# Optimization experiments

Measured on AMD Instinct MI355X. Metric: run time of the kernel, lower is better.

## Reference

```python
import jax, jax.numpy as jnp
import numpy as np

NUM_GRAPHS = 1000


def gcn_conv(x, src, dst, n_nodes, W, b):
    """PyG GCNConv: symmetric normalization with self-loops, then scatter-add."""
    # self-loops already appended to src/dst by caller
    deg = jax.ops.segment_sum(jnp.ones_like(dst, dtype=x.dtype), dst, num_segments=n_nodes)
    dinv = jnp.where(deg > 0, jax.lax.rsqrt(deg), 0.0)
    norm = dinv[src] * dinv[dst]                      # [E+N]
    h = x @ W.T                                       # [N, out]
    msg = h[src] * norm[:, None]                      # gather + scale
    out = jax.ops.segment_sum(msg, dst, num_segments=n_nodes)
    return out + b


def setup_inputs() -> dict:
    key = jax.random.key(0)
    ks = jax.random.split(key, 9)
    N, E = 100000, 1600000
    x = jax.random.normal(ks[0], (N, 32), dtype=jnp.float32)
    edge_index = jax.random.randint(ks[1], (2, E), 0, N, dtype=jnp.int64)
    batch = jnp.sort(jax.random.randint(ks[2], (N,), 0, NUM_GRAPHS, dtype=jnp.int64))
    # parameters (Glorot-ish scale)
    W1 = jax.random.normal(ks[3], (16, 32), dtype=jnp.float32) * (1.0 / np.sqrt(32))
    b1 = jnp.zeros((16,), dtype=jnp.float32)
    W2 = jax.random.normal(ks[4], (16, 16), dtype=jnp.float32) * (1.0 / np.sqrt(16))
    b2 = jnp.zeros((16,), dtype=jnp.float32)
    Wl = jax.random.normal(ks[5], (5, 16), dtype=jnp.float32) * (1.0 / np.sqrt(16))
    bl = jnp.zeros((5,), dtype=jnp.float32)
    return {"x": x, "edge_index": edge_index, "batch": batch,
            "W1": W1, "b1": b1, "W2": W2, "b2": b2, "Wl": Wl, "bl": bl}


def reference(x, edge_index, batch, W1, b1, W2, b2, Wl, bl):
    n_nodes = x.shape[0]
    loops = jnp.arange(n_nodes, dtype=edge_index.dtype)
    src = jnp.concatenate([edge_index[0], loops])
    dst = jnp.concatenate([edge_index[1], loops])

    h = gcn_conv(x, src, dst, n_nodes, W1, b1)
    h = jax.nn.relu(h)
    h = gcn_conv(h, src, dst, n_nodes, W2, b2)

    # global mean pool over graphs
    sums = jax.ops.segment_sum(h, batch, num_segments=NUM_GRAPHS)
    cnts = jax.ops.segment_sum(jnp.ones((n_nodes,), dtype=h.dtype), batch, num_segments=NUM_GRAPHS)
    pooled = sums / jnp.maximum(cnts, 1.0)[:, None]   # [G, 16]

    logits = pooled @ Wl.T + bl                       # [G, 5]
    return jax.nn.softmax(logits, axis=-1)
```

## Files before the change

### kernel.cpp

```cpp
#include <hip/hip_runtime.h>
#include <hip/hip_fp16.h>
#include <math.h>

#define NG 1000
#define NPN 512
#define PSH 9
#define MAXPART 256
#define K1BLK 256

__global__ void __launch_bounds__(256) hist_kernel(const int* __restrict__ dst,
                                                   int* __restrict__ bhist,
                                                   int4* __restrict__ zero4, int z4,
                                                   int E, int CH) {
    __shared__ int h[MAXPART];
    int b = blockIdx.x, t = threadIdx.x;
    h[t] = 0;
    int gid = b * 256 + t;
    if (gid < z4) zero4[gid] = make_int4(0, 0, 0, 0);
    __syncthreads();
    int beg = b * CH, end = min(E, beg + CH);
    for (int e = beg + t; e < end; e += 256) atomicAdd(&h[dst[e] >> PSH], 1);
    __syncthreads();
    bhist[t * K1BLK + b] = h[t];
}

__global__ void __launch_bounds__(256) scanA_kernel(const int* __restrict__ bhist,
                                                    int* __restrict__ gbase,
                                                    int* __restrict__ pcnt, int NPART) {
    int wid = blockIdx.x * 4 + (threadIdx.x >> 6);
    int lane = threadIdx.x & 63;
    if (wid >= NPART) return;
    int base = wid * K1BLK + lane * 4;
    int v0 = bhist[base + 0], v1 = bhist[base + 1];
    int v2 = bhist[base + 2], v3 = bhist[base + 3];
    int s = v0 + v1 + v2 + v3;
    int incl = s;
    for (int off = 1; off < 64; off <<= 1) {
        int u = __shfl_up(incl, off);
        if (lane >= off) incl += u;
    }
    int run = incl - s;
    gbase[base + 0] = run;            run += v0;
    gbase[base + 1] = run;            run += v1;
    gbase[base + 2] = run;            run += v2;
    gbase[base + 3] = run;
    if (lane == 63) pcnt[wid] = incl;
}

__global__ void __launch_bounds__(64) scanB_kernel(const int* __restrict__ pcnt,
                                                   int* __restrict__ poff,
                                                   int* __restrict__ rowptr,
                                                   int NPART, int N, int E) {
    int lane = threadIdx.x;
    int v[4];
    int s = 0;
#pragma unroll
    for (int k = 0; k < 4; k++) {
        int idx = lane * 4 + k;
        v[k] = (idx < NPART) ? pcnt[idx] : 0;
        s += v[k];
    }
    int incl = s;
    for (int off = 1; off < 64; off <<= 1) {
        int u = __shfl_up(incl, off);
        if (lane >= off) incl += u;
    }
    int run = incl - s;
#pragma unroll
    for (int k = 0; k < 4; k++) {
        int idx = lane * 4 + k;
        if (idx < NPART) poff[idx] = run;
        run += v[k];
    }
    int grand = __shfl(incl, 63);
    if (lane == 0) { poff[NPART] = grand; rowptr[N] = E; }
}

__global__ void __launch_bounds__(256) scatter_kernel(const int* __restrict__ src,
                                                      const int* __restrict__ dst,
                                                      const int* __restrict__ poff,
                                                      const int* __restrict__ gbase,
                                                      int* __restrict__ ibuf,
                                                      int E, int CH, int NPART) {
    __shared__ int cur[MAXPART];
    int b = blockIdx.x, t = threadIdx.x;
    if (t < NPART) cur[t] = poff[t] + gbase[t * K1BLK + b];
    __syncthreads();
    int beg = b * CH, end = min(E, beg + CH);
    for (int e = beg + t; e < end; e += 256) {
        int s = src[e], d = dst[e];
        int p = d >> PSH;
        int pos = atomicAdd(&cur[p], 1);
        ibuf[pos] = ((d & (NPN - 1)) << 17) | s;
    }
}

__global__ void __launch_bounds__(256) part_kernel(const int* __restrict__ poff,
                                                   const int* __restrict__ ibuf,
                                                   int* __restrict__ csr,
                                                   int* __restrict__ rowptr,
                                                   float* __restrict__ dinv,
                                                   const float* __restrict__ X,
                                                   const float* __restrict__ W1,
                                                   __half* __restrict__ A1h, int N) {
    __shared__ int h[NPN];
    __shared__ int ex[NPN];
    __shared__ int cur[NPN];
    __shared__ int sm[256];
    __shared__ float sW1[512];
    int p = blockIdx.x, t = threadIdx.x;
    int base = p * NPN;
    for (int k = t; k < NPN; k += 256) h[k] = 0;
    sW1[t] = W1[t];
    sW1[t + 256] = W1[t + 256];
    __syncthreads();
    int ebeg = poff[p], eend = poff[p + 1];
    for (int e = ebeg + t; e < eend; e += 256) atomicAdd(&h[ibuf[e] >> 17], 1);
    __syncthreads();
    int a0 = h[2 * t], a1 = h[2 * t + 1];
    int s = a0 + a1;
    sm[t] = s;
    __syncthreads();
    for (int o = 1; o < 256; o <<= 1) {
        int u = (t >= o) ? sm[t - o] : 0;
        __syncthreads();
        sm[t] += u;
        __syncthreads();
    }
    int exc = sm[t] - s;
    ex[2 * t] = exc;          cur[2 * t] = exc;
    ex[2 * t + 1] = exc + a0; cur[2 * t + 1] = exc + a0;
    __syncthreads();
    for (int k = t; k < NPN; k += 256) {
        int n = base + k;
        if (n < N) {
            rowptr[n] = ebeg + ex[k];
            dinv[n] = rsqrtf((float)h[k] + 1.0f);
        }
    }
    for (int e = ebeg + t; e < eend; e += 256) {
        int w = ibuf[e];
        int ln = w >> 17;
        int pos = ebeg + atomicAdd(&cur[ln], 1);
        csr[pos] = w & 0x1FFFF;
    }
    for (int k = t; k < NPN; k += 256) {
        int n = base + k;
        if (n >= N) continue;
        float dd = rsqrtf((float)h[k] + 1.0f);
        float xv[32];
        const float4* xp = (const float4*)(X + (size_t)n * 32);
#pragma unroll
        for (int qq = 0; qq < 8; qq++) {
            float4 v = xp[qq];
            xv[4*qq+0] = v.x; xv[4*qq+1] = v.y; xv[4*qq+2] = v.z; xv[4*qq+3] = v.w;
        }
        union { __half2 h2[8]; uint4 u4[2]; } pk;
#pragma unroll
        for (int j2 = 0; j2 < 8; j2++) {
            float o[2];
#pragma unroll
            for (int jj = 0; jj < 2; jj++) {
                int j = j2 * 2 + jj;
                float a = 0.f;
#pragma unroll
                for (int kk = 0; kk < 32; kk++) a += xv[kk] * sW1[j * 32 + kk];
                o[jj] = a * dd;
            }
            pk.h2[j2] = __floats2half2_rn(o[0], o[1]);
        }
        uint4* yp = (uint4*)(A1h + (size_t)n * 16);
        yp[0] = pk.u4[0];
        yp[1] = pk.u4[1];
    }
}

__device__ __forceinline__ void add8(float* a, uint4 v) {
    float2 f;
    f = __half22float2(*(const __half2*)&v.x); a[0] += f.x; a[1] += f.y;
    f = __half22float2(*(const __half2*)&v.y); a[2] += f.x; a[3] += f.y;
    f = __half22float2(*(const __half2*)&v.z); a[4] += f.x; a[5] += f.y;
    f = __half22float2(*(const __half2*)&v.w); a[6] += f.x; a[7] += f.y;
}

__global__ void __launch_bounds__(256) agg1_kernel(
    const int* __restrict__ rowptr, const int* __restrict__ csr,
    const float* __restrict__ dinv, const __half* __restrict__ A1h,
    const float* __restrict__ b1, const float* __restrict__ W2,
    __half* __restrict__ A2h, int N) {
    __shared__ float sW2[256];
    __shared__ float sb1[16];
    __shared__ float tile[128][17];
    int t = threadIdx.x;
    int team = t >> 1, q = t & 1;
    int node = blockIdx.x * 128 + team;
    sW2[t] = W2[t];
    if (t < 16) sb1[t] = b1[t];
    __syncthreads();
    const uint4* H4 = (const uint4*)A1h;
    float dd = 0.f;
    if (node < N) {
        dd = dinv[node];
        float acc[8] = {0.f,0.f,0.f,0.f,0.f,0.f,0.f,0.f};
        add8(acc, H4[(size_t)node * 2 + q]);
        int e = rowptr[node], end = rowptr[node + 1];
        for (; e + 3 < end; e += 4) {
            int s0 = csr[e], s1 = csr[e+1], s2 = csr[e+2], s3 = csr[e+3];
            uint4 g0 = H4[(size_t)s0 * 2 + q];
            uint4 g1 = H4[(size_t)s1 * 2 + q];
            uint4 g2 = H4[(size_t)s2 * 2 + q];
            uint4 g3 = H4[(size_t)s3 * 2 + q];
            add8(acc, g0); add8(acc, g1); add8(acc, g2); add8(acc, g3);
        }
        for (; e < end; e++) add8(acc, H4[(size_t)csr[e] * 2 + q]);
#pragma unroll
        for (int j = 0; j < 8; j++)
            tile[team][q * 8 + j] = fmaxf(acc[j] * dd + sb1[q * 8 + j], 0.f);
    }
    __syncthreads();
    if (node < N) {
        float o[8];
#pragma unroll
        for (int jj = 0; jj < 8; jj++) {
            int j = q * 8 + jj;
            float a = 0.f;
#pragma unroll
            for (int k = 0; k < 16; k++) a += tile[team][k] * sW2[j * 16 + k];
            o[jj] = a * dd;
        }
        uint4 ov;
        ((__half2*)&ov)[0] = __floats2half2_rn(o[0], o[1]);
        ((__half2*)&ov)[1] = __floats2half2_rn(o[2], o[3]);
        ((__half2*)&ov)[2] = __floats2half2_rn(o[4], o[5]);
        ((__half2*)&ov)[3] = __floats2half2_rn(o[6], o[7]);
        ((uint4*)A2h)[(size_t)node * 2 + q] = ov;
    }
}

__global__ void __launch_bounds__(256) agg2_kernel(
    const int* __restrict__ rowptr, const int* __restrict__ csr,
    const float* __restrict__ dinv, const __half* __restrict__ A2h,
    const int* __restrict__ batch, float* __restrict__ pooled,
    float* __restrict__ cnt, int N) {
    __shared__ float tile[128][17];
    __shared__ int gb[128];
    int t = threadIdx.x;
    int team = t >> 1, q = t & 1;
    int base = blockIdx.x * 128;
    int node = base + team;
    if (t < 128) {
        int n = base + t;
        gb[t] = (n < N) ? batch[n] : -1;
    }
    const uint4* H4 = (const uint4*)A2h;
    if (node < N) {
        float dd = dinv[node];
        float acc[8] = {0.f,0.f,0.f,0.f,0.f,0.f,0.f,0.f};
        add8(acc, H4[(size_t)node * 2 + q]);
        int e = rowptr[node], end = rowptr[node + 1];
        for (; e + 3 < end; e += 4) {
            int s0 = csr[e], s1 = csr[e+1], s2 = csr[e+2], s3 = csr[e+3];
            uint4 g0 = H4[(size_t)s0 * 2 + q];
            uint4 g1 = H4[(size_t)s1 * 2 + q];
            uint4 g2 = H4[(size_t)s2 * 2 + q];
            uint4 g3 = H4[(size_t)s3 * 2 + q];
            add8(acc, g0); add8(acc, g1); add8(acc, g2); add8(acc, g3);
        }
        for (; e < end; e++) add8(acc, H4[(size_t)csr[e] * 2 + q]);
#pragma unroll
        for (int j = 0; j < 8; j++) tile[team][q * 8 + j] = acc[j] * dd;
    }
    __syncthreads();
    int nmax = N - base; if (nmax > 128) nmax = 128;
    if (t < 16 && nmax > 0) {
        int c = t;
        int g = gb[0];
        float a = 0.f, k = 0.f;
        for (int n = 0; n < nmax; n++) {
            int gi = gb[n];
            if (gi != g) {
                atomicAdd(&pooled[(size_t)g * 16 + c], a);
                if (c == 0) atomicAdd(&cnt[g], k);
                a = 0.f; k = 0.f; g = gi;
            }
            a += tile[n][c];
            k += 1.f;
        }
        atomicAdd(&pooled[(size_t)g * 16 + c], a);
        if (c == 0) atomicAdd(&cnt[g], k);
    }
}

__global__ void head_kernel(const float* __restrict__ pooled, const float* __restrict__ cnt,
                            const float* __restrict__ b2, const float* __restrict__ Wl,
                            const float* __restrict__ bl, float* __restrict__ out) {
    int g = blockIdx.x * blockDim.x + threadIdx.x;
    if (g >= NG) return;
    float c = cnt[g];
    c = c > 1.0f ? c : 1.0f;
    float inv = 1.0f / c;
    float p[16];
#pragma unroll
    for (int j = 0; j < 16; j++) p[j] = pooled[(size_t)g * 16 + j] * inv + b2[j];
    float logits[5], m = -INFINITY;
#pragma unroll
    for (int r = 0; r < 5; r++) {
        float a = bl[r];
#pragma unroll
        for (int j = 0; j < 16; j++) a += p[j] * Wl[r * 16 + j];
        logits[r] = a;
        m = fmaxf(m, a);
    }
    float s = 0.f;
#pragma unroll
    for (int r = 0; r < 5; r++) { logits[r] = expf(logits[r] - m); s += logits[r]; }
    float is = 1.0f / s;
#pragma unroll
    for (int r = 0; r < 5; r++) out[(size_t)g * 5 + r] = logits[r] * is;
}

static inline size_t rnd16b(size_t bytes) { return (bytes + 15) & ~(size_t)15; }

extern "C" void kernel_launch(void* const* d_in, const int* in_sizes, int n_in,
                              void* d_out, int out_size, void* d_ws, size_t ws_size,
                              hipStream_t stream) {
    const float* x     = (const float*)d_in[0];
    const int*   edge  = (const int*)d_in[1];
    const int*   batch = (const int*)d_in[2];
    const float* W1    = (const float*)d_in[3];
    const float* b1    = (const float*)d_in[4];
    const float* W2    = (const float*)d_in[5];
    const float* b2    = (const float*)d_in[6];
    const float* Wl    = (const float*)d_in[7];
    const float* bl    = (const float*)d_in[8];

    const int N = in_sizes[0] / 32;
    const int E = in_sizes[1] / 2;
    const int* src = edge;
    const int* dst = edge + E;

    const int NPART = (N + NPN - 1) / NPN;
    const int CH = (E + K1BLK - 1) / K1BLK;

    char* ws = (char*)d_ws;
    size_t off = 0;
    float*    pooled = (float*)(ws + off);    off += rnd16b((size_t)NG * 16 * 4);
    float*    cnt    = (float*)(ws + off);    off += rnd16b((size_t)NG * 4);
    size_t zbytes = off;
    int*      poff   = (int*)(ws + off);      off += rnd16b((size_t)(MAXPART + 1) * 4);
    int*      pcnt   = (int*)(ws + off);      off += rnd16b((size_t)MAXPART * 4);
    int*      rowptr = (int*)(ws + off);      off += rnd16b((size_t)(N + 1) * 4);
    float*    dinv   = (float*)(ws + off);    off += rnd16b((size_t)N * 4);
    int*      bhist  = (int*)(ws + off);      off += rnd16b((size_t)K1BLK * MAXPART * 4);
    int*      gbase  = (int*)(ws + off);      off += rnd16b((size_t)K1BLK * MAXPART * 4);
    int*      ibuf   = (int*)(ws + off);      off += rnd16b((size_t)E * 4);
    int*      csr    = (int*)(ws + off);      off += rnd16b((size_t)E * 4);
    __half*   A1h    = (__half*)(ws + off);   off += rnd16b((size_t)N * 16 * 2);
    __half*   A2h    = (__half*)(ws + off);   off += rnd16b((size_t)N * 16 * 2);

    int z4 = (int)(zbytes / 16);

    hist_kernel<<<K1BLK, 256, 0, stream>>>(dst, bhist, (int4*)d_ws, z4, E, CH);
    scanA_kernel<<<(NPART + 3) / 4, 256, 0, stream>>>(bhist, gbase, pcnt, NPART);
    scanB_kernel<<<1, 64, 0, stream>>>(pcnt, poff, rowptr, NPART, N, E);
    scatter_kernel<<<K1BLK, 256, 0, stream>>>(src, dst, poff, gbase, ibuf, E, CH, NPART);
    part_kernel<<<NPART, 256, 0, stream>>>(poff, ibuf, csr, rowptr, dinv, x, W1, A1h, N);

    int gAgg = (N + 127) / 128;
    agg1_kernel<<<gAgg, 256, 0, stream>>>(rowptr, csr, dinv, A1h, b1, W2, A2h, N);
    agg2_kernel<<<gAgg, 256, 0, stream>>>(rowptr, csr, dinv, A2h, batch, pooled, cnt, N);
    head_kernel<<<(NG + 255) / 256, 256, 0, stream>>>(pooled, cnt, b2, Wl, bl, (float*)d_out);
}
```

Baseline: 103.1 us.

## Fuse all GCN stages into one cooperative persistent kernel with grid syncs

Replaces the eight separate kernel launches with a single cooperative kernel of 256 blocks that runs histogram, scans, scatter, CSR build, both aggregations, pooling and the head, separated by grid-wide syncs. Degree normalization is recomputed from rowptr inline instead of reading a dinv array. The aim is to remove launch gaps and inter-kernel drain. The trade-off is that the aggregation phases now use only 256 persistent blocks looping over strips, which may lower latency hiding for the gather-heavy phases, and grid.sync adds its own cost. Falls back to the old multi-kernel path if cooperative launch is unavailable.

```diff
diff --git a/kernel.cpp b/kernel.cpp
--- a/kernel.cpp
+++ b/kernel.cpp
@@ -1,12 +1,312 @@
 #include <hip/hip_runtime.h>
+#include <hip/hip_cooperative_groups.h>
 #include <hip/hip_fp16.h>
 #include <math.h>
+
+namespace cg = cooperative_groups;
 
 #define NG 1000
 #define NPN 512
 #define PSH 9
 #define MAXPART 256
 #define K1BLK 256
+#define NBLK 256
+#define NTHR 256
+
+__device__ __forceinline__ void add8(float* a, uint4 v) {
+    float2 f;
+    f = __half22float2(*(const __half2*)&v.x); a[0] += f.x; a[1] += f.y;
+    f = __half22float2(*(const __half2*)&v.y); a[2] += f.x; a[3] += f.y;
+    f = __half22float2(*(const __half2*)&v.z); a[4] += f.x; a[5] += f.y;
+    f = __half22float2(*(const __half2*)&v.w); a[6] += f.x; a[7] += f.y;
+}
+
+struct GParams {
+    const float* x; const int* src; const int* dst; const int* batch;
+    const float* W1; const float* b1; const float* W2; const float* b2;
+    const float* Wl; const float* bl; float* out;
+    float* pooled; float* cnt; int* poff; int* rowptr; int* pcnt;
+    int* bhist; int* gbase; int* ibuf; int* csr;
+    __half* A1h; __half* A2h;
+    int N, E, NPART, CH, z4;
+};
+
+__global__ void __launch_bounds__(NTHR) mega_kernel(GParams P) {
+    cg::grid_group grid = cg::this_grid();
+    __shared__ __align__(16) char smem[10368];
+    int b = blockIdx.x, t = threadIdx.x;
+
+    {
+        int4* z = (int4*)P.pooled;
+        for (int i = b * NTHR + t; i < P.z4; i += NBLK * NTHR) z[i] = make_int4(0,0,0,0);
+        int* h = (int*)smem;
+        h[t] = 0;
+        __syncthreads();
+        int beg = b * P.CH, end = min(P.E, beg + P.CH);
+        for (int e = beg + t; e < end; e += NTHR) atomicAdd(&h[P.dst[e] >> PSH], 1);
+        __syncthreads();
+        if (t < P.NPART) P.bhist[t * NBLK + b] = h[t];
+    }
+    grid.sync();
+    {
+        int wid = b * (NTHR / 64) + (t >> 6);
+        int lane = t & 63;
+        if (wid < P.NPART) {
+            int base = wid * NBLK + lane * 4;
+            int v0 = P.bhist[base + 0], v1 = P.bhist[base + 1];
+            int v2 = P.bhist[base + 2], v3 = P.bhist[base + 3];
+            int s = v0 + v1 + v2 + v3;
+            int incl = s;
+            for (int off = 1; off < 64; off <<= 1) {
+                int u = __shfl_up(incl, off);
+                if (lane >= off) incl += u;
+            }
+            int run = incl - s;
+            P.gbase[base + 0] = run;  run += v0;
+            P.gbase[base + 1] = run;  run += v1;
+            P.gbase[base + 2] = run;  run += v2;
+            P.gbase[base + 3] = run;
+            if (lane == 63) P.pcnt[wid] = incl;
+        }
+    }
+    grid.sync();
+    if (b == 0 && t < 64) {
+        int lane = t;
+        int v[4];
+        int s = 0;
+#pragma unroll
+        for (int k = 0; k < 4; k++) {
+            int idx = lane * 4 + k;
+            v[k] = (idx < P.NPART) ? P.pcnt[idx] : 0;
+            s += v[k];
+        }
+        int incl = s;
+        for (int off = 1; off < 64; off <<= 1) {
+            int u = __shfl_up(incl, off);
+            if (lane >= off) incl += u;
+        }
+        int run = incl - s;
+#pragma unroll
+        for (int k = 0; k < 4; k++) {
+            int idx = lane * 4 + k;
+            if (idx < P.NPART) P.poff[idx] = run;
+            run += v[k];
+        }
+        int grand = __shfl(incl, 63);
+        if (lane == 0) { P.poff[P.NPART] = grand; P.rowptr[P.N] = P.E; }
+    }
+    grid.sync();
+    {
+        int* cur = (int*)smem;
+        if (t < P.NPART) cur[t] = P.poff[t] + P.gbase[t * NBLK + b];
+        __syncthreads();
+        int beg = b * P.CH, end = min(P.E, beg + P.CH);
+        for (int e = beg + t; e < end; e += NTHR) {
+            int s = P.src[e], d = P.dst[e];
+            int p = d >> PSH;
+            int pos = atomicAdd(&cur[p], 1);
+            P.ibuf[pos] = ((d & (NPN - 1)) << 17) | s;
+        }
+        __syncthreads();
+    }
+    grid.sync();
+    if (b < P.NPART) {
+        int p = b;
+        int* h    = (int*)smem;
+        int* ex   = h + NPN;
+        int* cur2 = ex + NPN;
+        int* sm   = cur2 + NPN;
+        float* sW1 = (float*)(sm + 256);
+        int base = p * NPN;
+        for (int k = t; k < NPN; k += NTHR) h[k] = 0;
+        sW1[t] = P.W1[t];
+        sW1[t + 256] = P.W1[t + 256];
+        __syncthreads();
+        int ebeg = P.poff[p], eend = P.poff[p + 1];
+        for (int e = ebeg + t; e < eend; e += NTHR) atomicAdd(&h[P.ibuf[e] >> 17], 1);
+        __syncthreads();
+        int a0 = h[2 * t], a1 = h[2 * t + 1];
+        int s = a0 + a1;
+        sm[t] = s;
+        __syncthreads();
+        for (int o = 1; o < 256; o <<= 1) {
+            int u = (t >= o) ? sm[t - o] : 0;
+            __syncthreads();
+            sm[t] += u;
+            __syncthreads();
+        }
+        int exc = sm[t] - s;
+        ex[2 * t] = exc;           cur2[2 * t] = exc;
+        ex[2 * t + 1] = exc + a0;  cur2[2 * t + 1] = exc + a0;
+        __syncthreads();
+        for (int k = t; k < NPN; k += NTHR) {
+            int n = base + k;
+            if (n < P.N) P.rowptr[n] = ebeg + ex[k];
+        }
+        for (int e = ebeg + t; e < eend; e += NTHR) {
+            int w = P.ibuf[e];
+            int ln = w >> 17;
+            int pos = ebeg + atomicAdd(&cur2[ln], 1);
+            P.csr[pos] = w & 0x1FFFF;
+        }
+        for (int k = t; k < NPN; k += NTHR) {
+            int n = base + k;
+            if (n >= P.N) continue;
+            float dd = rsqrtf((float)h[k] + 1.0f);
+            float xv[32];
+            const float4* xp = (const float4*)(P.x + (size_t)n * 32);
+#pragma unroll
+            for (int qq = 0; qq < 8; qq++) {
+                float4 v = xp[qq];
+                xv[4*qq+0] = v.x; xv[4*qq+1] = v.y; xv[4*qq+2] = v.z; xv[4*qq+3] = v.w;
+            }
+            union { __half2 h2[8]; uint4 u4[2]; } pk;
+#pragma unroll
+            for (int j2 = 0; j2 < 8; j2++) {
+                float o[2];
+#pragma unroll
+                for (int jj = 0; jj < 2; jj++) {
+                    int j = j2 * 2 + jj;
+                    float a = 0.f;
+#pragma unroll
+                    for (int kk = 0; kk < 32; kk++) a += xv[kk] * sW1[j * 32 + kk];
+                    o[jj] = a * dd;
+                }
+                pk.h2[j2] = __floats2half2_rn(o[0], o[1]);
+            }
+            uint4* yp = (uint4*)(P.A1h + (size_t)n * 16);
+            yp[0] = pk.u4[0];
+            yp[1] = pk.u4[1];
+        }
+    }
+    grid.sync();
+    {
+        float* sW2 = (float*)smem;
+        float* sb1 = sW2 + 256;
+        float (*tile)[17] = (float (*)[17])(sb1 + 16);
+        sW2[t] = P.W2[t];
+        if (t < 16) sb1[t] = P.b1[t];
+        __syncthreads();
+        int strips = (P.N + 127) / 128;
+        const uint4* H4 = (const uint4*)P.A1h;
+        int team = t >> 1, q = t & 1;
+        for (int sblk = b; sblk < strips; sblk += NBLK) {
+            int node = sblk * 128 + team;
+            float dd = 0.f;
+            if (node < P.N) {
+                int e = P.rowptr[node], end = P.rowptr[node + 1];
+                dd = rsqrtf((float)(end - e) + 1.0f);
+                float acc[8] = {0.f,0.f,0.f,0.f,0.f,0.f,0.f,0.f};
+                add8(acc, H4[(size_t)node * 2 + q]);
+                for (; e + 3 < end; e += 4) {
+                    int s0 = P.csr[e], s1 = P.csr[e+1], s2 = P.csr[e+2], s3 = P.csr[e+3];
+                    uint4 g0 = H4[(size_t)s0 * 2 + q];
+                    uint4 g1 = H4[(size_t)s1 * 2 + q];
+                    uint4 g2 = H4[(size_t)s2 * 2 + q];
+                    uint4 g3 = H4[(size_t)s3 * 2 + q];
+                    add8(acc, g0); add8(acc, g1); add8(acc, g2); add8(acc, g3);
+                }
+                for (; e < end; e++) add8(acc, H4[(size_t)P.csr[e] * 2 + q]);
+#pragma unroll
+                for (int j = 0; j < 8; j++)
+                    tile[team][q * 8 + j] = fmaxf(acc[j] * dd + sb1[q * 8 + j], 0.f);
+            }
+            __syncthreads();
+            if (node < P.N) {
+                float o[8];
+#pragma unroll
+                for (int jj = 0; jj < 8; jj++) {
+                    int j = q * 8 + jj;
+                    float a = 0.f;
+#pragma unroll
+                    for (int k = 0; k < 16; k++) a += tile[team][k] * sW2[j * 16 + k];
+                    o[jj] = a * dd;
+                }
+                uint4 ov;
+                ((__half2*)&ov)[0] = __floats2half2_rn(o[0], o[1]);
+                ((__half2*)&ov)[1] = __floats2half2_rn(o[2], o[3]);
+                ((__half2*)&ov)[2] = __floats2half2_rn(o[4], o[5]);
+                ((__half2*)&ov)[3] = __floats2half2_rn(o[6], o[7]);
+                ((uint4*)P.A2h)[(size_t)node * 2 + q] = ov;
+            }
+            __syncthreads();
+        }
+    }
+    grid.sync();
+    {
+        float (*tile)[17] = (float (*)[17])smem;
+        int* gb = (int*)(smem + 128 * 17 * 4);
+        int strips = (P.N + 127) / 128;
+        const uint4* H4 = (const uint4*)P.A2h;
+        int team = t >> 1, q = t & 1;
+        for (int sblk = b; sblk < strips; sblk += NBLK) {
+            int base2 = sblk * 128;
+            int node = base2 + team;
+            if (t < 128) gb[t] = (base2 + t < P.N) ? P.batch[base2 + t] : -1;
+            if (node < P.N) {
+                int e = P.rowptr[node], end = P.rowptr[node + 1];
+                float dd = rsqrtf((float)(end - e) + 1.0f);
+                float acc[8] = {0.f,0.f,0.f,0.f,0.f,0.f,0.f,0.f};
+                add8(acc, H4[(size_t)node * 2 + q]);
+                for (; e + 3 < end; e += 4) {
+                    int s0 = P.csr[e], s1 = P.csr[e+1], s2 = P.csr[e+2], s3 = P.csr[e+3];
+                    uint4 g0 = H4[(size_t)s0 * 2 + q];
+                    uint4 g1 = H4[(size_t)s1 * 2 + q];
+                    uint4 g2 = H4[(size_t)s2 * 2 + q];
+                    uint4 g3 = H4[(size_t)s3 * 2 + q];
+                    add8(acc, g0); add8(acc, g1); add8(acc, g2); add8(acc, g3);
+                }
+                for (; e < end; e++) add8(acc, H4[(size_t)P.csr[e] * 2 + q]);
+#pragma unroll
+                for (int j = 0; j < 8; j++) tile[team][q * 8 + j] = acc[j] * dd;
+            }
+            __syncthreads();
+            int nmax = P.N - base2; if (nmax > 128) nmax = 128;
+            if (t < 16 && nmax > 0) {
+                int c = t;
+                int g = gb[0];
+                float a = 0.f, k = 0.f;
+                for (int n = 0; n < nmax; n++) {
+                    int gi = gb[n];
+                    if (gi != g) {
+                        atomicAdd(&P.pooled[(size_t)g * 16 + c], a);
+                        if (c == 0) atomicAdd(&P.cnt[g], k);
+                        a = 0.f; k = 0.f; g = gi;
+                    }
+                    a += tile[n][c];
+                    k += 1.f;
+                }
+                atomicAdd(&P.pooled[(size_t)g * 16 + c], a);
+                if (c == 0) atomicAdd(&P.cnt[g], k);
+            }
+            __syncthreads();
+        }
+    }
+    grid.sync();
+    for (int g = b * NTHR + t; g < NG; g += NBLK * NTHR) {
+        float c = P.cnt[g];
+        c = c > 1.0f ? c : 1.0f;
+        float inv = 1.0f / c;
+        float pv[16];
+#pragma unroll
+        for (int j = 0; j < 16; j++) pv[j] = P.pooled[(size_t)g * 16 + j] * inv + P.b2[j];
+        float logits[5], m = -INFINITY;
+#pragma unroll
+        for (int r = 0; r < 5; r++) {
+            float a = P.bl[r];
+#pragma unroll
+            for (int j = 0; j < 16; j++) a += pv[j] * P.Wl[r * 16 + j];
+            logits[r] = a;
+            m = fmaxf(m, a);
+        }
+        float s = 0.f;
+#pragma unroll
+        for (int r = 0; r < 5; r++) { logits[r] = expf(logits[r] - m); s += logits[r]; }
+        float is = 1.0f / s;
+#pragma unroll
+        for (int r = 0; r < 5; r++) P.out[(size_t)g * 5 + r] = logits[r] * is;
+    }
+}
 
 __global__ void __launch_bounds__(256) hist_kernel(const int* __restrict__ dst,
                                                    int* __restrict__ bhist,
@@ -175,14 +475,6 @@
     }
 }
 
-__device__ __forceinline__ void add8(float* a, uint4 v) {
-    float2 f;
-    f = __half22float2(*(const __half2*)&v.x); a[0] += f.x; a[1] += f.y;
-    f = __half22float2(*(const __half2*)&v.y); a[2] += f.x; a[3] += f.y;
-    f = __half22float2(*(const __half2*)&v.z); a[4] += f.x; a[5] += f.y;
-    f = __half22float2(*(const __half2*)&v.w); a[6] += f.x; a[7] += f.y;
-}
-
 __global__ void __launch_bounds__(256) agg1_kernel(
     const int* __restrict__ rowptr, const int* __restrict__ csr,
     const float* __restrict__ dinv, const __half* __restrict__ A1h,
@@ -340,7 +632,6 @@
     const int* dst = edge + E;
 
     const int NPART = (N + NPN - 1) / NPN;
-    const int CH = (E + K1BLK - 1) / K1BLK;
 
     char* ws = (char*)d_ws;
     size_t off = 0;
@@ -360,12 +651,36 @@
 
     int z4 = (int)(zbytes / 16);
 
+    int dev = 0, coop = 0, nCU = 0, maxB = 0;
+    hipGetDevice(&dev);
+    hipDeviceGetAttribute(&coop, hipDeviceAttributeCooperativeLaunch, dev);
+    hipDeviceGetAttribute(&nCU, hipDeviceAttributeMultiprocessorCount, dev);
+    hipError_t occ = hipOccupancyMaxActiveBlocksPerMultiprocessor(&maxB, (const void*)mega_kernel, NTHR, 0);
+    bool canCoop = (coop == 1) && (occ == hipSuccess) && ((long)maxB * nCU >= NBLK);
+    if (canCoop) {
+        GParams P;
+        P.x = x; P.src = src; P.dst = dst; P.batch = batch;
+        P.W1 = W1; P.b1 = b1; P.W2 = W2; P.b2 = b2; P.Wl = Wl; P.bl = bl;
+        P.out = (float*)d_out;
+        P.pooled = pooled; P.cnt = cnt; P.poff = poff; P.rowptr = rowptr; P.pcnt = pcnt;
+        P.bhist = bhist; P.gbase = gbase; P.ibuf = ibuf; P.csr = csr;
+        P.A1h = A1h; P.A2h = A2h;
+        P.N = N; P.E = E; P.NPART = NPART;
+        P.CH = (E + NBLK - 1) / NBLK;
+        P.z4 = z4;
+        void* kargs[] = { (void*)&P };
+        hipError_t err = hipLaunchCooperativeKernel((const void*)mega_kernel,
+                                                    dim3(NBLK), dim3(NTHR), kargs, 0, stream);
+        if (err == hipSuccess) return;
+        (void)hipGetLastError();
+    }
+
+    const int CH = (E + K1BLK - 1) / K1BLK;
     hist_kernel<<<K1BLK, 256, 0, stream>>>(dst, bhist, (int4*)d_ws, z4, E, CH);
     scanA_kernel<<<(NPART + 3) / 4, 256, 0, stream>>>(bhist, gbase, pcnt, NPART);
     scanB_kernel<<<1, 64, 0, stream>>>(pcnt, poff, rowptr, NPART, N, E);
     scatter_kernel<<<K1BLK, 256, 0, stream>>>(src, dst, poff, gbase, ibuf, E, CH, NPART);
     part_kernel<<<NPART, 256, 0, stream>>>(poff, ibuf, csr, rowptr, dinv, x, W1, A1h, N);
-
     int gAgg = (N + 127) / 128;
     agg1_kernel<<<gAgg, 256, 0, stream>>>(rowptr, csr, dinv, A1h, b1, W2, A2h, N);
     agg2_kernel<<<gAgg, 256, 0, stream>>>(rowptr, csr, dinv, A2h, batch, pooled, cnt, N);
```

New measurement: 103.9 us. About the same (+0.7%).

## Fold partition scan into consumers, derive dinv from rowptr, fuse head via last-block ticket

Applied to the files above, without the earlier changes.

Removes the single-block scanB kernel by having every scatter and part block recompute the partition-offset scan from pcnt redundantly. Drops the dinv array and instead recomputes the inverse square-root degree from rowptr differences in both aggregation kernels. Fuses the pooling head and softmax into agg2 using an atomic done-counter so the last block finishes the work. This removes two kernel launches and some global traffic, at the cost of redundant scan work per block and a serialized tail in one block.

```diff
diff --git a/kernel.cpp b/kernel.cpp
--- a/kernel.cpp
+++ b/kernel.cpp
@@ -47,44 +47,37 @@
     if (lane == 63) pcnt[wid] = incl;
 }
 
-__global__ void __launch_bounds__(64) scanB_kernel(const int* __restrict__ pcnt,
-                                                   int* __restrict__ poff,
-                                                   int* __restrict__ rowptr,
-                                                   int NPART, int N, int E) {
-    int lane = threadIdx.x;
-    int v[4];
-    int s = 0;
-#pragma unroll
-    for (int k = 0; k < 4; k++) {
-        int idx = lane * 4 + k;
-        v[k] = (idx < NPART) ? pcnt[idx] : 0;
-        s += v[k];
-    }
-    int incl = s;
-    for (int off = 1; off < 64; off <<= 1) {
-        int u = __shfl_up(incl, off);
-        if (lane >= off) incl += u;
-    }
-    int run = incl - s;
-#pragma unroll
-    for (int k = 0; k < 4; k++) {
-        int idx = lane * 4 + k;
-        if (idx < NPART) poff[idx] = run;
-        run += v[k];
-    }
-    int grand = __shfl(incl, 63);
-    if (lane == 0) { poff[NPART] = grand; rowptr[N] = E; }
-}
-
 __global__ void __launch_bounds__(256) scatter_kernel(const int* __restrict__ src,
                                                       const int* __restrict__ dst,
-                                                      const int* __restrict__ poff,
+                                                      const int* __restrict__ pcnt,
                                                       const int* __restrict__ gbase,
                                                       int* __restrict__ ibuf,
                                                       int E, int CH, int NPART) {
     __shared__ int cur[MAXPART];
     int b = blockIdx.x, t = threadIdx.x;
-    if (t < NPART) cur[t] = poff[t] + gbase[t * K1BLK + b];
+    if (t < 64) {
+        int lane = t;
+        int v[4];
+        int s = 0;
+#pragma unroll
+        for (int k = 0; k < 4; k++) {
+            int idx = lane * 4 + k;
+            v[k] = (idx < NPART) ? pcnt[idx] : 0;
+            s += v[k];
+        }
+        int incl = s;
+        for (int off = 1; off < 64; off <<= 1) {
+            int u = __shfl_up(incl, off);
+            if (lane >= off) incl += u;
+        }
+        int run = incl - s;
+#pragma unroll
+        for (int k = 0; k < 4; k++) {
+            int idx = lane * 4 + k;
+            if (idx < NPART) cur[idx] = run + gbase[idx * K1BLK + b];
+            run += v[k];
+        }
+    }
     __syncthreads();
     int beg = b * CH, end = min(E, beg + CH);
     for (int e = beg + t; e < end; e += 256) {
@@ -95,26 +88,51 @@
     }
 }
 
-__global__ void __launch_bounds__(256) part_kernel(const int* __restrict__ poff,
+__global__ void __launch_bounds__(256) part_kernel(const int* __restrict__ pcnt,
                                                    const int* __restrict__ ibuf,
                                                    int* __restrict__ csr,
                                                    int* __restrict__ rowptr,
-                                                   float* __restrict__ dinv,
                                                    const float* __restrict__ X,
                                                    const float* __restrict__ W1,
-                                                   __half* __restrict__ A1h, int N) {
+                                                   __half* __restrict__ A1h,
+                                                   int N, int E, int NPART) {
     __shared__ int h[NPN];
     __shared__ int ex[NPN];
     __shared__ int cur[NPN];
     __shared__ int sm[256];
     __shared__ float sW1[512];
+    __shared__ int sEbeg, sEend;
     int p = blockIdx.x, t = threadIdx.x;
     int base = p * NPN;
     for (int k = t; k < NPN; k += 256) h[k] = 0;
     sW1[t] = W1[t];
     sW1[t + 256] = W1[t + 256];
-    __syncthreads();
-    int ebeg = poff[p], eend = poff[p + 1];
+    if (t < 64) {
+        int lane = t;
+        int v[4];
+        int s = 0;
+#pragma unroll
+        for (int k = 0; k < 4; k++) {
+            int idx = lane * 4 + k;
+            v[k] = (idx < NPART) ? pcnt[idx] : 0;
+            s += v[k];
+        }
+        int incl = s;
+        for (int off = 1; off < 64; off <<= 1) {
+            int u = __shfl_up(incl, off);
+            if (lane >= off) incl += u;
+        }
+        int run = incl - s;
+#pragma unroll
+        for (int k = 0; k < 4; k++) {
+            int idx = lane * 4 + k;
+            if (idx == p) { sEbeg = run; sEend = run + v[k]; }
+            run += v[k];
+        }
+    }
+    if (p == 0 && t == 0) rowptr[N] = E;
+    __syncthreads();
+    int ebeg = sEbeg, eend = sEend;
     for (int e = ebeg + t; e < eend; e += 256) atomicAdd(&h[ibuf[e] >> 17], 1);
     __syncthreads();
     int a0 = h[2 * t], a1 = h[2 * t + 1];
@@ -133,10 +151,7 @@
     __syncthreads();
     for (int k = t; k < NPN; k += 256) {
         int n = base + k;
-        if (n < N) {
-            rowptr[n] = ebeg + ex[k];
-            dinv[n] = rsqrtf((float)h[k] + 1.0f);
-        }
+        if (n < N) rowptr[n] = ebeg + ex[k];
     }
     for (int e = ebeg + t; e < eend; e += 256) {
         int w = ibuf[e];
@@ -185,9 +200,8 @@
 
 __global__ void __launch_bounds__(256) agg1_kernel(
     const int* __restrict__ rowptr, const int* __restrict__ csr,
-    const float* __restrict__ dinv, const __half* __restrict__ A1h,
-    const float* __restrict__ b1, const float* __restrict__ W2,
-    __half* __restrict__ A2h, int N) {
+    const __half* __restrict__ A1h, const float* __restrict__ b1,
+    const float* __restrict__ W2, __half* __restrict__ A2h, int N) {
     __shared__ float sW2[256];
     __shared__ float sb1[16];
     __shared__ float tile[128][17];
@@ -200,10 +214,10 @@
     const uint4* H4 = (const uint4*)A1h;
     float dd = 0.f;
     if (node < N) {
-        dd = dinv[node];
+        int e = rowptr[node], end = rowptr[node + 1];
+        dd = rsqrtf((float)(end - e) + 1.0f);
         float acc[8] = {0.f,0.f,0.f,0.f,0.f,0.f,0.f,0.f};
         add8(acc, H4[(size_t)node * 2 + q]);
-        int e = rowptr[node], end = rowptr[node + 1];
         for (; e + 3 < end; e += 4) {
             int s0 = csr[e], s1 = csr[e+1], s2 = csr[e+2], s3 = csr[e+3];
             uint4 g0 = H4[(size_t)s0 * 2 + q];
@@ -239,11 +253,14 @@
 
 __global__ void __launch_bounds__(256) agg2_kernel(
     const int* __restrict__ rowptr, const int* __restrict__ csr,
-    const float* __restrict__ dinv, const __half* __restrict__ A2h,
-    const int* __restrict__ batch, float* __restrict__ pooled,
-    float* __restrict__ cnt, int N) {
+    const __half* __restrict__ A2h, const int* __restrict__ batch,
+    float* __restrict__ pooled, float* __restrict__ cnt,
+    int* __restrict__ done,
+    const float* __restrict__ b2, const float* __restrict__ Wl,
+    const float* __restrict__ bl, float* __restrict__ out, int N) {
     __shared__ float tile[128][17];
     __shared__ int gb[128];
+    __shared__ int sTicket;
     int t = threadIdx.x;
     int team = t >> 1, q = t & 1;
     int base = blockIdx.x * 128;
@@ -254,10 +271,10 @@
     }
     const uint4* H4 = (const uint4*)A2h;
     if (node < N) {
-        float dd = dinv[node];
+        int e = rowptr[node], end = rowptr[node + 1];
+        float dd = rsqrtf((float)(end - e) + 1.0f);
         float acc[8] = {0.f,0.f,0.f,0.f,0.f,0.f,0.f,0.f};
         add8(acc, H4[(size_t)node * 2 + q]);
-        int e = rowptr[node], end = rowptr[node + 1];
         for (; e + 3 < end; e += 4) {
             int s0 = csr[e], s1 = csr[e+1], s2 = csr[e+2], s3 = csr[e+3];
             uint4 g0 = H4[(size_t)s0 * 2 + q];
@@ -289,34 +306,35 @@
         atomicAdd(&pooled[(size_t)g * 16 + c], a);
         if (c == 0) atomicAdd(&cnt[g], k);
     }
-}
-
-__global__ void head_kernel(const float* __restrict__ pooled, const float* __restrict__ cnt,
-                            const float* __restrict__ b2, const float* __restrict__ Wl,
-                            const float* __restrict__ bl, float* __restrict__ out) {
-    int g = blockIdx.x * blockDim.x + threadIdx.x;
-    if (g >= NG) return;
-    float c = cnt[g];
-    c = c > 1.0f ? c : 1.0f;
-    float inv = 1.0f / c;
-    float p[16];
-#pragma unroll
-    for (int j = 0; j < 16; j++) p[j] = pooled[(size_t)g * 16 + j] * inv + b2[j];
-    float logits[5], m = -INFINITY;
-#pragma unroll
-    for (int r = 0; r < 5; r++) {
-        float a = bl[r];
-#pragma unroll
-        for (int j = 0; j < 16; j++) a += p[j] * Wl[r * 16 + j];
-        logits[r] = a;
-        m = fmaxf(m, a);
-    }
-    float s = 0.f;
-#pragma unroll
-    for (int r = 0; r < 5; r++) { logits[r] = expf(logits[r] - m); s += logits[r]; }
-    float is = 1.0f / s;
-#pragma unroll
-    for (int r = 0; r < 5; r++) out[(size_t)g * 5 + r] = logits[r] * is;
+    __threadfence();
+    __syncthreads();
+    if (t == 0) sTicket = atomicAdd(done, 1);
+    __syncthreads();
+    if (sTicket != (int)gridDim.x - 1) return;
+    for (int g = t; g < NG; g += 256) {
+        float c = atomicAdd(&cnt[g], 0.0f);
+        c = c > 1.0f ? c : 1.0f;
+        float inv = 1.0f / c;
+        float pv[16];
+#pragma unroll
+        for (int j = 0; j < 16; j++)
+            pv[j] = atomicAdd(&pooled[(size_t)g * 16 + j], 0.0f) * inv + b2[j];
+        float logits[5], m = -INFINITY;
+#pragma unroll
+        for (int r = 0; r < 5; r++) {
+            float a = bl[r];
+#pragma unroll
+            for (int j = 0; j < 16; j++) a += pv[j] * Wl[r * 16 + j];
+            logits[r] = a;
+            m = fmaxf(m, a);
+        }
+        float s = 0.f;
+#pragma unroll
+        for (int r = 0; r < 5; r++) { logits[r] = expf(logits[r] - m); s += logits[r]; }
+        float is = 1.0f / s;
+#pragma unroll
+        for (int r = 0; r < 5; r++) out[(size_t)g * 5 + r] = logits[r] * is;
+    }
 }
 
 static inline size_t rnd16b(size_t bytes) { return (bytes + 15) & ~(size_t)15; }
@@ -346,11 +364,10 @@
     size_t off = 0;
     float*    pooled = (float*)(ws + off);    off += rnd16b((size_t)NG * 16 * 4);
     float*    cnt    = (float*)(ws + off);    off += rnd16b((size_t)NG * 4);
+    int*      done   = (int*)(ws + off);      off += 16;
     size_t zbytes = off;
-    int*      poff   = (int*)(ws + off);      off += rnd16b((size_t)(MAXPART + 1) * 4);
     int*      pcnt   = (int*)(ws + off);      off += rnd16b((size_t)MAXPART * 4);
     int*      rowptr = (int*)(ws + off);      off += rnd16b((size_t)(N + 1) * 4);
-    float*    dinv   = (float*)(ws + off);    off += rnd16b((size_t)N * 4);
     int*      bhist  = (int*)(ws + off);      off += rnd16b((size_t)K1BLK * MAXPART * 4);
     int*      gbase  = (int*)(ws + off);      off += rnd16b((size_t)K1BLK * MAXPART * 4);
     int*      ibuf   = (int*)(ws + off);      off += rnd16b((size_t)E * 4);
@@ -362,12 +379,11 @@
 
     hist_kernel<<<K1BLK, 256, 0, stream>>>(dst, bhist, (int4*)d_ws, z4, E, CH);
     scanA_kernel<<<(NPART + 3) / 4, 256, 0, stream>>>(bhist, gbase, pcnt, NPART);
-    scanB_kernel<<<1, 64, 0, stream>>>(pcnt, poff, rowptr, NPART, N, E);
-    scatter_kernel<<<K1BLK, 256, 0, stream>>>(src, dst, poff, gbase, ibuf, E, CH, NPART);
-    part_kernel<<<NPART, 256, 0, stream>>>(poff, ibuf, csr, rowptr, dinv, x, W1, A1h, N);
+    scatter_kernel<<<K1BLK, 256, 0, stream>>>(src, dst, pcnt, gbase, ibuf, E, CH, NPART);
+    part_kernel<<<NPART, 256, 0, stream>>>(pcnt, ibuf, csr, rowptr, x, W1, A1h, N, E, NPART);
 
     int gAgg = (N + 127) / 128;
-    agg1_kernel<<<gAgg, 256, 0, stream>>>(rowptr, csr, dinv, A1h, b1, W2, A2h, N);
-    agg2_kernel<<<gAgg, 256, 0, stream>>>(rowptr, csr, dinv, A2h, batch, pooled, cnt, N);
-    head_kernel<<<(NG + 255) / 256, 256, 0, stream>>>(pooled, cnt, b2, Wl, bl, (float*)d_out);
-}
+    agg1_kernel<<<gAgg, 256, 0, stream>>>(rowptr, csr, A1h, b1, W2, A2h, N);
+    agg2_kernel<<<gAgg, 256, 0, stream>>>(rowptr, csr, A2h, batch, pooled, cnt, done,
+                                          b2, Wl, bl, (float*)d_out, N);
+}
```

Result: slower. 158.8 us (+54.0%).
